# Kernel tuning notes

Measured on AMD Instinct MI355X. Metric: run time of the kernel, lower is better.

The kernel has to match this reference:

```python
import math
import jax, jax.numpy as jnp
import numpy as np

WINDOW_SHAPE = [30, 30, 8]
DEPTH = 8
NUM_DIMS = 3
N_POINTS = 2_000_000
BATCH = 4
SPARSE_SHAPE = np.array([32, 512, 512], dtype=np.int64)  # [D, H, W]


def _right_shift_bits(b, k):
    # shift bit-array right along last axis: prepend k zeros, drop last k
    if b.shape[-1] <= k:
        return jnp.zeros_like(b)
    pad = [(0, 0)] * (b.ndim - 1) + [(k, 0)]
    return jnp.pad(b[..., :-k], pad)


def _gray2binary(gray):
    # prefix-XOR along last axis via doubling (matches torch gray2binary)
    n = gray.shape[-1]
    shift = 2 ** (math.ceil(math.log2(n)) - 1)
    while shift > 0:
        gray = jnp.logical_xor(gray, _right_shift_bits(gray, shift))
        shift //= 2
    return gray


def hilbert_encode(locs, num_dims, num_bits):
    # locs: [N, num_dims] int, each in [0, 2**num_bits)
    n = locs.shape[0]
    # bit b of gray is the (num_bits-1-b)-th bit of the coordinate (MSB first)
    shifts_ = (num_bits - 1 - jnp.arange(num_bits, dtype=locs.dtype))
    gray = ((locs[:, :, None] >> shifts_[None, None, :]) & 1).astype(bool)  # [N, D, B]
    # Skilling's transform: small fixed loop (num_bits*num_dims = 24 iters)
    for bit in range(num_bits):
        for dim in range(num_dims):
            mask = gray[:, dim, bit]  # [N]
            g0 = jnp.logical_xor(gray[:, 0, bit + 1:], mask[:, None])
            gray = gray.at[:, 0, bit + 1:].set(g0)
            to_flip = jnp.logical_and(
                jnp.logical_not(mask)[:, None],
                jnp.logical_xor(gray[:, 0, bit + 1:], gray[:, dim, bit + 1:]),
            )
            gray = gray.at[:, dim, bit + 1:].set(
                jnp.logical_xor(gray[:, dim, bit + 1:], to_flip))
            gray = gray.at[:, 0, bit + 1:].set(
                jnp.logical_xor(gray[:, 0, bit + 1:], to_flip))
    # interleave: swapaxes(1,2) then flatten -> [N, num_bits*num_dims], MSB first
    bits = jnp.transpose(gray, (0, 2, 1)).reshape(n, num_bits * num_dims)
    hb = _gray2binary(bits)
    nb = num_bits * num_dims
    weights = jnp.asarray((1 << (nb - 1 - np.arange(nb))), dtype=jnp.int32)
    code = (hb.astype(jnp.int32) * weights).sum(-1)
    return code


def setup_inputs() -> dict:
    key = jax.random.key(0)
    kb, kz, ky, kx = jax.random.split(key, 4)
    D, H, W = [int(v) for v in SPARSE_SHAPE]
    b = jax.random.randint(kb, (N_POINTS,), 0, BATCH, dtype=jnp.int32)
    z = jax.random.randint(kz, (N_POINTS,), 0, D, dtype=jnp.int32)
    y = jax.random.randint(ky, (N_POINTS,), 0, H, dtype=jnp.int32)
    x = jax.random.randint(kx, (N_POINTS,), 0, W, dtype=jnp.int32)
    coords = jnp.stack([b, z, y, x], axis=-1)  # [N, 4]: bs, z, y, x
    return {"coords": coords, "sparse_shape": SPARSE_SHAPE, "shifts": 1}


def reference(coords, sparse_shape, shifts):
    # sparse_shape is static config: [D, H, W]; reversed -> W, H, D (as in torch)
    ss = [int(v) for v in np.asarray(sparse_shape)][::-1]
    W, H, D = ss
    wx, wy, wz = WINDOW_SHAPE
    if bool(shifts):
        sx, sy, sz = math.ceil(wx / 2), math.ceil(wy / 2), math.ceil(wz / 2)
    else:
        sx = sy = sz = 0
    b = coords[:, 0]
    x = (coords[:, 3] + sx) % W
    y = (coords[:, 2] + sy) % H
    z = (coords[:, 1] + sz) % D
    locs = jnp.stack([x, y, z], axis=-1)  # [N, 3]
    code = hilbert_encode(locs, NUM_DIMS, DEPTH)
    code = code | (b.astype(code.dtype) << (DEPTH * 3))
    coords2curve = jnp.argsort(code)
    return coords2curve
```

## Files before the change

### kernel.cpp

```cpp
#include <hip/hip_runtime.h>
#include <stdint.h>


#define THREADS 512
#define TILE 4096
#define ROUNDS (TILE / THREADS)
#define WAVES (THREADS / 64)
#define CHUNK (TILE / WAVES)

__device__ __forceinline__ int tile_of(int bid, int nwg) {
  int q = nwg >> 3, r = nwg & 7;
  int x = bid & 7, k = bid >> 3;
  return x * q + (x < r ? x : r) + k;
}

__device__ __forceinline__ uint32_t hilbert_code(uint32_t x, uint32_t y, uint32_t z) {
  uint32_t X0 = x & 255u, X1 = y & 255u, X2 = z & 255u;
#pragma unroll
  for (int p = 7; p >= 0; --p) {
    uint32_t low = (1u << p) - 1u;
    uint32_t f0 = (uint32_t)-(int)((X0 >> p) & 1u);
    X0 ^= (low & f0);
    uint32_t f1 = (uint32_t)-(int)((X1 >> p) & 1u);
    uint32_t t1 = ((X0 ^ X1) & low) & ~f1;
    X0 ^= (low & f1) ^ t1;
    X1 ^= t1;
    uint32_t f2 = (uint32_t)-(int)((X2 >> p) & 1u);
    uint32_t t2 = ((X0 ^ X2) & low) & ~f2;
    X0 ^= (low & f2) ^ t2;
    X2 ^= t2;
  }
  uint32_t G = 0;
#pragma unroll
  for (int k = 0; k < 8; ++k) {
    int p = 7 - k;
    G |= ((X0 >> p) & 1u) << (23 - 3 * k);
    G |= ((X1 >> p) & 1u) << (22 - 3 * k);
    G |= ((X2 >> p) & 1u) << (21 - 3 * k);
  }
  G ^= G >> 16; G ^= G >> 8; G ^= G >> 4; G ^= G >> 2; G ^= G >> 1;
  return G & 0xFFFFFFu;
}

__global__ __launch_bounds__(THREADS) void genkeys_hist(
    const int4* __restrict__ coords, const void* __restrict__ ss,
    const int* __restrict__ shifts, uint64_t* __restrict__ pairs,
    int* __restrict__ hist, int N) {
  __shared__ int lh[512];
  int t = threadIdx.x, b = tile_of(blockIdx.x, gridDim.x);
  lh[t] = 0;

  const int* p32 = (const int*)ss;
  int D, H, W;
  if (p32[1] == 0) { const long long* p64 = (const long long*)ss;
    D = (int)p64[0]; H = (int)p64[1]; W = (int)p64[2]; }
  else { D = p32[0]; H = p32[1]; W = p32[2]; }
  int sflag = shifts[0];
  int sx = sflag ? 15 : 0, sy = sflag ? 15 : 0, sz = sflag ? 4 : 0;
  bool wp2 = (W & (W - 1)) == 0, hp2 = (H & (H - 1)) == 0, dp2 = (D & (D - 1)) == 0;
  __syncthreads();

#pragma unroll
  for (int r = 0; r < ROUNDS; ++r) {
    int idx = b * TILE + r * THREADS + t;
    if (idx < N) {
      int4 c = coords[idx];
      uint32_t bb = (uint32_t)c.x;
      int zz = c.y + sz, yy = c.z + sy, xx = c.w + sx;
      uint32_t z = (uint32_t)(dp2 ? (zz & (D - 1)) : (zz % D));
      uint32_t y = (uint32_t)(hp2 ? (yy & (H - 1)) : (yy % H));
      uint32_t x = (uint32_t)(wp2 ? (xx & (W - 1)) : (xx % W));
      uint32_t code = hilbert_code(x, y, z) | (bb << 24);
      pairs[idx] = ((uint64_t)(uint32_t)idx << 32) | code;
      atomicAdd(&lh[code & 511u], 1);
    }
  }
  __syncthreads();
  hist[(size_t)b * 512 + t] = lh[t];
}

template <int SHIFT, int NB>
__global__ __launch_bounds__(THREADS) void hist_kernel(
    const uint64_t* __restrict__ pairs, int* __restrict__ hist, int N) {
  __shared__ int lh[NB];
  int t = threadIdx.x, b = tile_of(blockIdx.x, gridDim.x);
  if (t < NB) lh[t] = 0;
  __syncthreads();
  const uint32_t* keys = (const uint32_t*)pairs;
#pragma unroll
  for (int r = 0; r < ROUNDS; ++r) {
    int idx = b * TILE + r * THREADS + t;
    if (idx < N) atomicAdd(&lh[(keys[(size_t)idx * 2] >> SHIFT) & (NB - 1)], 1);
  }
  __syncthreads();
  if (t < NB) hist[(size_t)b * NB + t] = lh[t];
}

__global__ __launch_bounds__(512) void scan_blocks(
    int* __restrict__ hist, int* __restrict__ digitTotals, int nblocks, int nbins) {
  __shared__ int wsum[8];
  int d = blockIdx.x, t = threadIdx.x, wave = t >> 6, lane = t & 63;
  int carry = 0;
  for (int start = 0; start < nblocks; start += 512) {
    int i = start + t;
    int vv = (i < nblocks) ? hist[(size_t)i * nbins + d] : 0;
    int x = vv;
#pragma unroll
    for (int off = 1; off < 64; off <<= 1) {
      int n = __shfl_up(x, off);
      if (lane >= off) x += n;
    }
    if (lane == 63) wsum[wave] = x;
    __syncthreads();
    int pre = 0;
    for (int w = 0; w < wave; ++w) pre += wsum[w];
    if (i < nblocks) hist[(size_t)i * nbins + d] = carry + pre + x - vv;
    int tot = 0;
    for (int w = 0; w < 8; ++w) tot += wsum[w];
    __syncthreads();
    carry += tot;
  }
  if (t == 0) digitTotals[d] = carry;
}

template <int SHIFT, int NB, bool FINAL>
__global__ __launch_bounds__(THREADS) void scatter_kernel(
    const uint64_t* __restrict__ pairsIn,
    uint64_t* __restrict__ pairsOut, int* __restrict__ valsOut,
    const int* __restrict__ hist, const int* __restrict__ digitTotals,
    int N) {
  constexpr int RB = (NB == 512) ? 9 : 8;
  __shared__ uint64_t sbuf[FINAL ? TILE / 2 : TILE];
  __shared__ __align__(16) unsigned short cnt[WAVES][NB];
  int t = threadIdx.x, b = tile_of(blockIdx.x, gridDim.x);
  int wave = t >> 6, lane = t & 63;

  int histv = 0, dt = 0;
  if (t < NB) {
    histv = hist[(size_t)b * NB + t];
    dt = digitTotals[t];
  }
  for (int i = t; i < WAVES * NB; i += THREADS) ((unsigned short*)cnt)[i] = 0;
  __syncthreads();

  uint64_t kvR[ROUNDS];
  int drR[ROUNDS];
  uint64_t ltm = (1ull << lane) - 1ull;
  int chunk0 = b * TILE + wave * CHUNK;

#pragma unroll
  for (int r = 0; r < ROUNDS; ++r) {
    int idx = chunk0 + r * 64 + lane;
    bool valid = idx < N;
    uint64_t kv = valid ? pairsIn[idx] : 0ull;
    kvR[r] = kv;
    int digit = (int)(((uint32_t)kv >> SHIFT) & (NB - 1));
    uint64_t eq = __ballot(valid);
#pragma unroll
    for (int bit = 0; bit < RB; ++bit) {
      uint64_t m = __ballot((digit >> bit) & 1);
      eq &= ((digit >> bit) & 1) ? m : ~m;
    }
    int waveRank = __popcll(eq & ltm);
    int cntW = __popcll(eq);
    int prior = cnt[wave][digit];
    drR[r] = valid ? (digit | ((prior + waveRank) << RB)) : -1;
    if (valid && waveRank == 0) cnt[wave][digit] = (unsigned short)(prior + cntW);
  }
  __syncthreads();

  int2* wt = (int2*)sbuf;
  int tot = 0, adjv = 0;
  int2 v = make_int2(0, 0);
  if (t < NB) {
#pragma unroll
    for (int w = 0; w < WAVES; ++w) tot += cnt[w][t];
    v = make_int2(tot, dt);
#pragma unroll
    for (int off = 1; off < 64; off <<= 1) {
      int nx = __shfl_up(v.x, off), ny = __shfl_up(v.y, off);
      if (lane >= off) { v.x += nx; v.y += ny; }
    }
    if (lane == 63) wt[wave] = v;
  }
  __syncthreads();
  if (t < NB) {
    int2 pre = make_int2(0, 0);
    for (int w = 0; w < wave; ++w) { pre.x += wt[w].x; pre.y += wt[w].y; }
    int ds = pre.x + v.x - tot;
    adjv = histv + (pre.y + v.y - dt) - ds;
    int run = ds;
#pragma unroll
    for (int w = 0; w < WAVES; ++w) {
      int x = cnt[w][t];
      cnt[w][t] = (unsigned short)run;
      run += x;
    }
  }
  __syncthreads();

#pragma unroll
  for (int r = 0; r < ROUNDS; ++r) {
    int dr = drR[r];
    if (dr >= 0) {
      int digit = dr & (NB - 1);
      int rnk = dr >> RB;
      int slot = (int)cnt[wave][digit] + rnk;
      if (FINAL)
        ((uint32_t*)sbuf)[slot] = ((uint32_t)digit << 23) | (uint32_t)(kvR[r] >> 32);
      else
        sbuf[slot] = kvR[r];
    }
  }
  __syncthreads();

  int* adjArr = (int*)cnt;
  if (t < NB) adjArr[t] = adjv;
  __syncthreads();

  int validCount = min(TILE, N - b * TILE);
#pragma unroll
  for (int j = 0; j < ROUNDS; ++j) {
    int i = j * THREADS + t;
    if (i < validCount) {
      if (FINAL) {
        uint32_t pk = ((uint32_t*)sbuf)[i];
        int digit = (int)(pk >> 23);
        valsOut[adjArr[digit] + i] = (int)(pk & 0x7FFFFFu);
      } else {
        uint64_t kv = sbuf[i];
        int digit = (int)(((uint32_t)kv >> SHIFT) & (NB - 1));
        pairsOut[adjArr[digit] + i] = kv;
      }
    }
  }
}

extern "C" void kernel_launch(void* const* d_in, const int* in_sizes, int n_in,
                              void* d_out, int out_size, void* d_ws, size_t ws_size,
                              hipStream_t stream) {
  const int4* coords = (const int4*)d_in[0];
  const void* ss = d_in[1];
  const int* shifts = (const int*)d_in[2];
  int N = in_sizes[0] / 4;
  int nblocks = (N + TILE - 1) / TILE;

  char* ws = (char*)d_ws;
  size_t off = 0;
  auto alloc = [&](size_t bytes) -> void* {
    void* p = ws + off;
    off += (bytes + 255) & ~(size_t)255;
    return p;
  };
  uint64_t* pairsA = (uint64_t*)alloc((size_t)N * 8);
  uint64_t* pairsB = (uint64_t*)alloc((size_t)N * 8);
  int*      hist   = (int*)alloc((size_t)512 * nblocks * 4);
  int*      digitTotals = (int*)alloc(512 * 4);

  genkeys_hist<<<nblocks, THREADS, 0, stream>>>(coords, ss, shifts, pairsA, hist, N);
  scan_blocks<<<512, 512, 0, stream>>>(hist, digitTotals, nblocks, 512);
  scatter_kernel<0, 512, false><<<nblocks, THREADS, 0, stream>>>(
      pairsA, pairsB, nullptr, hist, digitTotals, N);

  hist_kernel<9, 512><<<nblocks, THREADS, 0, stream>>>(pairsB, hist, N);
  scan_blocks<<<512, 512, 0, stream>>>(hist, digitTotals, nblocks, 512);
  scatter_kernel<9, 512, false><<<nblocks, THREADS, 0, stream>>>(
      pairsB, pairsA, nullptr, hist, digitTotals, N);

  hist_kernel<18, 256><<<nblocks, THREADS, 0, stream>>>(pairsA, hist, N);
  scan_blocks<<<256, 512, 0, stream>>>(hist, digitTotals, nblocks, 256);
  scatter_kernel<18, 256, true><<<nblocks, THREADS, 0, stream>>>(
      pairsA, nullptr, (int*)d_out, hist, digitTotals, N);
}
```

Measured before the change: 85.02 us.

## Split radix sort pairs into 32-bit key/value arrays and pack last pass

The radix sort no longer stores interleaved 64-bit key/index pairs. The first pass reads 32-bit keys only and generates indices on the fly. Pass two writes a single packed 32-bit word holding the top key bits and a 22-bit index, so the third pass moves only 4 bytes per element. This cuts global memory traffic across the sort passes. It relies on N fitting in 22 bits and the remaining key bits fitting in 10 bits.

```diff
diff --git a/kernel.cpp b/kernel.cpp
--- a/kernel.cpp
+++ b/kernel.cpp
@@ -7,6 +7,8 @@
 #define ROUNDS (TILE / THREADS)
 #define WAVES (THREADS / 64)
 #define CHUNK (TILE / WAVES)
+#define IDX_BITS 22
+#define IDX_MASK 0x3FFFFFu
 
 __device__ __forceinline__ int tile_of(int bid, int nwg) {
   int q = nwg >> 3, r = nwg & 7;
@@ -44,7 +46,7 @@
 
 __global__ __launch_bounds__(THREADS) void genkeys_hist(
     const int4* __restrict__ coords, const void* __restrict__ ss,
-    const int* __restrict__ shifts, uint64_t* __restrict__ pairs,
+    const int* __restrict__ shifts, uint32_t* __restrict__ keys0,
     int* __restrict__ hist, int N) {
   __shared__ int lh[512];
   int t = threadIdx.x, b = tile_of(blockIdx.x, gridDim.x);
@@ -71,7 +73,7 @@
       uint32_t y = (uint32_t)(hp2 ? (yy & (H - 1)) : (yy % H));
       uint32_t x = (uint32_t)(wp2 ? (xx & (W - 1)) : (xx % W));
       uint32_t code = hilbert_code(x, y, z) | (bb << 24);
-      pairs[idx] = ((uint64_t)(uint32_t)idx << 32) | code;
+      keys0[idx] = code;
       atomicAdd(&lh[code & 511u], 1);
     }
   }
@@ -81,16 +83,15 @@
 
 template <int SHIFT, int NB>
 __global__ __launch_bounds__(THREADS) void hist_kernel(
-    const uint64_t* __restrict__ pairs, int* __restrict__ hist, int N) {
+    const uint32_t* __restrict__ keys, int* __restrict__ hist, int N) {
   __shared__ int lh[NB];
   int t = threadIdx.x, b = tile_of(blockIdx.x, gridDim.x);
   if (t < NB) lh[t] = 0;
   __syncthreads();
-  const uint32_t* keys = (const uint32_t*)pairs;
 #pragma unroll
   for (int r = 0; r < ROUNDS; ++r) {
     int idx = b * TILE + r * THREADS + t;
-    if (idx < N) atomicAdd(&lh[(keys[(size_t)idx * 2] >> SHIFT) & (NB - 1)], 1);
+    if (idx < N) atomicAdd(&lh[(keys[idx] >> SHIFT) & (NB - 1)], 1);
   }
   __syncthreads();
   if (t < NB) hist[(size_t)b * NB + t] = lh[t];
@@ -123,14 +124,15 @@
   if (t == 0) digitTotals[d] = carry;
 }
 
-template <int SHIFT, int NB, bool FINAL>
+template <int MODE>
 __global__ __launch_bounds__(THREADS) void scatter_kernel(
-    const uint64_t* __restrict__ pairsIn,
-    uint64_t* __restrict__ pairsOut, int* __restrict__ valsOut,
-    const int* __restrict__ hist, const int* __restrict__ digitTotals,
-    int N) {
-  constexpr int RB = (NB == 512) ? 9 : 8;
-  __shared__ uint64_t sbuf[FINAL ? TILE / 2 : TILE];
+    const uint32_t* __restrict__ in0, const uint32_t* __restrict__ in1,
+    uint32_t* __restrict__ out0, uint32_t* __restrict__ out1,
+    const int* __restrict__ hist, const int* __restrict__ digitTotals, int N) {
+  constexpr int NB = (MODE == 2) ? 256 : 512;
+  constexpr int RB = (MODE == 2) ? 8 : 9;
+  constexpr int SHIFT = (MODE == 0) ? 0 : (MODE == 1) ? 9 : 22;
+  __shared__ uint64_t sbuf[(MODE == 2) ? TILE / 2 : TILE];
   __shared__ __align__(16) unsigned short cnt[WAVES][NB];
   int t = threadIdx.x, b = tile_of(blockIdx.x, gridDim.x);
   int wave = t >> 6, lane = t & 63;
@@ -152,9 +154,13 @@
   for (int r = 0; r < ROUNDS; ++r) {
     int idx = chunk0 + r * 64 + lane;
     bool valid = idx < N;
-    uint64_t kv = valid ? pairsIn[idx] : 0ull;
+    uint32_t a = valid ? in0[idx] : 0u;
+    uint64_t kv;
+    if (MODE == 0)      kv = ((uint64_t)(uint32_t)idx << 32) | a;
+    else if (MODE == 1) kv = ((uint64_t)(valid ? in1[idx] : 0u) << 32) | a;
+    else                kv = a;
     kvR[r] = kv;
-    int digit = (int)(((uint32_t)kv >> SHIFT) & (NB - 1));
+    int digit = (int)((a >> SHIFT) & (NB - 1));
     uint64_t eq = __ballot(valid);
 #pragma unroll
     for (int bit = 0; bit < RB; ++bit) {
@@ -206,10 +212,8 @@
       int digit = dr & (NB - 1);
       int rnk = dr >> RB;
       int slot = (int)cnt[wave][digit] + rnk;
-      if (FINAL)
-        ((uint32_t*)sbuf)[slot] = ((uint32_t)digit << 23) | (uint32_t)(kvR[r] >> 32);
-      else
-        sbuf[slot] = kvR[r];
+      if (MODE == 2) ((uint32_t*)sbuf)[slot] = (uint32_t)kvR[r];
+      else           sbuf[slot] = kvR[r];
     }
   }
   __syncthreads();
@@ -223,14 +227,21 @@
   for (int j = 0; j < ROUNDS; ++j) {
     int i = j * THREADS + t;
     if (i < validCount) {
-      if (FINAL) {
-        uint32_t pk = ((uint32_t*)sbuf)[i];
-        int digit = (int)(pk >> 23);
-        valsOut[adjArr[digit] + i] = (int)(pk & 0x7FFFFFu);
+      if (MODE == 0) {
+        uint64_t kv = sbuf[i];
+        uint32_t key = (uint32_t)kv;
+        int pos = adjArr[key & 511u] + i;
+        out0[pos] = key;
+        out1[pos] = (uint32_t)(kv >> 32);
+      } else if (MODE == 1) {
+        uint64_t kv = sbuf[i];
+        uint32_t key = (uint32_t)kv, idxv = (uint32_t)(kv >> 32);
+        int pos = adjArr[(key >> 9) & 511u] + i;
+        out0[pos] = ((key >> 18) << IDX_BITS) | idxv;
       } else {
-        uint64_t kv = sbuf[i];
-        int digit = (int)(((uint32_t)kv >> SHIFT) & (NB - 1));
-        pairsOut[adjArr[digit] + i] = kv;
+        uint32_t p = ((uint32_t*)sbuf)[i];
+        int pos = adjArr[(p >> IDX_BITS) & 255u] + i;
+        out0[pos] = p & IDX_MASK;
       }
     }
   }
@@ -252,23 +263,25 @@
     off += (bytes + 255) & ~(size_t)255;
     return p;
   };
-  uint64_t* pairsA = (uint64_t*)alloc((size_t)N * 8);
-  uint64_t* pairsB = (uint64_t*)alloc((size_t)N * 8);
-  int*      hist   = (int*)alloc((size_t)512 * nblocks * 4);
+  uint32_t* keys0 = (uint32_t*)alloc((size_t)N * 4);
+  uint32_t* keys1 = (uint32_t*)alloc((size_t)N * 4);
+  uint32_t* vals1 = (uint32_t*)alloc((size_t)N * 4);
+  uint32_t* packd = (uint32_t*)alloc((size_t)N * 4);
+  int*      hist  = (int*)alloc((size_t)512 * nblocks * 4);
   int*      digitTotals = (int*)alloc(512 * 4);
 
-  genkeys_hist<<<nblocks, THREADS, 0, stream>>>(coords, ss, shifts, pairsA, hist, N);
+  genkeys_hist<<<nblocks, THREADS, 0, stream>>>(coords, ss, shifts, keys0, hist, N);
   scan_blocks<<<512, 512, 0, stream>>>(hist, digitTotals, nblocks, 512);
-  scatter_kernel<0, 512, false><<<nblocks, THREADS, 0, stream>>>(
-      pairsA, pairsB, nullptr, hist, digitTotals, N);
-
-  hist_kernel<9, 512><<<nblocks, THREADS, 0, stream>>>(pairsB, hist, N);
+  scatter_kernel<0><<<nblocks, THREADS, 0, stream>>>(
+      keys0, nullptr, keys1, vals1, hist, digitTotals, N);
+
+  hist_kernel<9, 512><<<nblocks, THREADS, 0, stream>>>(keys1, hist, N);
   scan_blocks<<<512, 512, 0, stream>>>(hist, digitTotals, nblocks, 512);
-  scatter_kernel<9, 512, false><<<nblocks, THREADS, 0, stream>>>(
-      pairsB, pairsA, nullptr, hist, digitTotals, N);
-
-  hist_kernel<18, 256><<<nblocks, THREADS, 0, stream>>>(pairsA, hist, N);
+  scatter_kernel<1><<<nblocks, THREADS, 0, stream>>>(
+      keys1, vals1, packd, nullptr, hist, digitTotals, N);
+
+  hist_kernel<22, 256><<<nblocks, THREADS, 0, stream>>>(packd, hist, N);
   scan_blocks<<<256, 512, 0, stream>>>(hist, digitTotals, nblocks, 256);
-  scatter_kernel<18, 256, true><<<nblocks, THREADS, 0, stream>>>(
-      pairsA, nullptr, (int*)d_out, hist, digitTotals, N);
-}
+  scatter_kernel<2><<<nblocks, THREADS, 0, stream>>>(
+      packd, nullptr, (uint32_t*)d_out, nullptr, hist, digitTotals, N);
+}
```

Result: faster. 82.60 us (-2.8%).
